# Kernel optimization log

Hardware: AMD Instinct MI355X
Metric: run time of the kernel (lower is better)

## Reference

```python
import jax, jax.numpy as jnp
import numpy as np

N, IN_DIM, OUT_DIM, HEADS = 50000, 256, 256, 8
C = OUT_DIM // HEADS  # per-head channels = 32
E = 800000
G = 64  # number of graphs in the batch
NEG_SLOPE = 0.2
GN_EPS = 1e-5


def setup_inputs() -> dict:
    key = jax.random.key(0)
    ks = jax.random.split(key, 12)
    x = jax.random.normal(ks[0], (N, IN_DIM), dtype=jnp.float32)
    edge_index = jax.random.randint(ks[1], (2, E), 0, N, dtype=jnp.int64)
    batch = jnp.sort(jax.random.randint(ks[2], (N,), 0, G, dtype=jnp.int64))
    s = 1.0 / np.sqrt(IN_DIM)
    W_l = jax.random.uniform(ks[3], (IN_DIM, HEADS * C), jnp.float32, -s, s)
    b_l = jnp.zeros((HEADS * C,), jnp.float32)
    W_r = jax.random.uniform(ks[4], (IN_DIM, HEADS * C), jnp.float32, -s, s)
    b_r = jnp.zeros((HEADS * C,), jnp.float32)
    att = jax.random.normal(ks[5], (HEADS, C), dtype=jnp.float32) / np.sqrt(C)
    bias = jnp.zeros((HEADS * C,), jnp.float32)
    gn_weight = jnp.ones((OUT_DIM,), jnp.float32)
    gn_bias = jnp.zeros((OUT_DIM,), jnp.float32)
    gn_mean_scale = jnp.ones((OUT_DIM,), jnp.float32)
    return {"x": x, "edge_index": edge_index, "batch": batch,
            "W_l": W_l, "b_l": b_l, "W_r": W_r, "b_r": b_r,
            "att": att, "bias": bias, "gn_weight": gn_weight,
            "gn_bias": gn_bias, "gn_mean_scale": gn_mean_scale}


def _gat_block(x, src, dst, batch, W_l, b_l, W_r, b_r, att, bias,
               gn_weight, gn_bias, gn_mean_scale):
    n = x.shape[0]
    # GATv2Conv (add_self_loops=True, concat=True)
    loops = jnp.arange(n, dtype=src.dtype)
    src = jnp.concatenate([src, loops])
    dst = jnp.concatenate([dst, loops])
    xl = (x @ W_l + b_l).reshape(n, HEADS, C)  # source transform
    xr = (x @ W_r + b_r).reshape(n, HEADS, C)  # target transform
    e = jax.nn.leaky_relu(xl[src] + xr[dst], NEG_SLOPE)  # [E', H, C]
    logits = jnp.einsum('ehc,hc->eh', e, att)            # [E', H]
    # segment softmax over incoming edges of each destination node
    m = jax.ops.segment_max(logits, dst, num_segments=n)
    alpha = jnp.exp(logits - m[dst])
    denom = jax.ops.segment_sum(alpha, dst, num_segments=n)
    alpha = alpha / (denom[dst] + 1e-16)
    msg = xl[src] * alpha[:, :, None]                    # [E', H, C]
    h = jax.ops.segment_sum(msg, dst, num_segments=n).reshape(n, HEADS * C) + bias
    # identity residual (in_dim == out_dim) + ELU
    h = jax.nn.elu(h + x)
    # GraphNorm (post-norm)
    counts = jnp.maximum(jax.ops.segment_sum(jnp.ones((n,), h.dtype), batch,
                                             num_segments=G), 1.0)
    mean = jax.ops.segment_sum(h, batch, num_segments=G) / counts[:, None]
    out0 = h - gn_mean_scale * mean[batch]
    var = jax.ops.segment_sum(out0 * out0, batch, num_segments=G) / counts[:, None]
    return gn_weight * out0 / jnp.sqrt(var[batch] + GN_EPS) + gn_bias


def reference(x, edge_index, batch, W_l, b_l, W_r, b_r, att, bias,
              gn_weight, gn_bias, gn_mean_scale):
    return _gat_block(x, edge_index[0], edge_index[1], batch,
                      W_l, b_l, W_r, b_r, att, bias,
                      gn_weight, gn_bias, gn_mean_scale)
```

## Files before the change

kernel.cpp:

```cpp
#include <hip/hip_runtime.h>
#include <hip/hip_bf16.h>
#include <stdint.h>

#define N_NODES 50000
#define MPAD    50048
#define IN_DIM  256
#define EDGES   800000
#define EPRIME  (EDGES + N_NODES)
#define NGRAPH  64
#define GN_EPS  1e-5f
#define ECPAD   53248
#define NBLK    208

typedef __attribute__((ext_vector_type(8))) short short8;
typedef __attribute__((ext_vector_type(4))) float floatx4;
typedef __attribute__((ext_vector_type(2))) float float2v;

__device__ __forceinline__ uint32_t pk2bf(float a, float b) {
    union { __hip_bfloat162 h; uint32_t u; } cv;
    cv.h = __float22bfloat162_rn(make_float2(a, b));
    return cv.u;
}

__device__ __forceinline__ unsigned short f2b(float f) {
    uint32_t u = __float_as_uint(f);
    u += 0x7fffu + ((u >> 16) & 1u);
    return (unsigned short)(u >> 16);
}

__global__ __launch_bounds__(256) void k_prep_w(const float* __restrict__ Wl,
                                                const float* __restrict__ Wr,
                                                unsigned short* __restrict__ Wt) {
    int idx = blockIdx.x * 256 + threadIdx.x;
    int n = idx >> 8, k = idx & 255;
    float v = (n < 256) ? Wl[k * 256 + n] : Wr[k * 256 + (n - 256)];
    Wt[idx] = f2b(v);
}

__global__ __launch_bounds__(512) void k_gemm(const float* __restrict__ x,
                                              const unsigned short* __restrict__ Wt,
                                              const float* __restrict__ bl,
                                              const float* __restrict__ br,
                                              unsigned short* __restrict__ XL,
                                              unsigned short* __restrict__ XR) {
    __shared__ unsigned short As[64 * 256];
    int rbase = blockIdx.x * 64;
    int tid = threadIdx.x;

#pragma unroll
    for (int it = 0; it < 4; ++it) {
        int c = it * 512 + tid;
        int row = c >> 5, ch = c & 31;
        int gr = rbase + row;
        float4 f0, f1;
        if (gr < N_NODES) {
            const float4* src = (const float4*)(x + (size_t)gr * 256 + ch * 8);
            f0 = src[0]; f1 = src[1];
        } else {
            f0 = make_float4(0.f,0.f,0.f,0.f); f1 = f0;
        }
        uint32_t p0 = pk2bf(f0.x, f0.y), p1 = pk2bf(f0.z, f0.w);
        uint32_t p2 = pk2bf(f1.x, f1.y), p3 = pk2bf(f1.z, f1.w);
        uint4 hv = make_uint4(p0, p1, p2, p3);
        *(uint4*)(As + row * 256 + (ch ^ (row & 7)) * 8) = hv;
    }
    __syncthreads();

    int w = tid >> 6;
    int l = tid & 63;
    int m = l & 15, q = l >> 4;

    floatx4 acc[4][4];
#pragma unroll
    for (int rf = 0; rf < 4; ++rf)
#pragma unroll
        for (int cf = 0; cf < 4; ++cf)
            acc[rf][cf] = (floatx4){0.f, 0.f, 0.f, 0.f};

    const unsigned short* wbase = Wt + (size_t)(w * 64) * 256;

#pragma unroll
    for (int kk = 0; kk < 8; ++kk) {
        short8 a[4];
#pragma unroll
        for (int rf = 0; rf < 4; ++rf) {
            int row = rf * 16 + m;
            int ch = (kk * 4 + q) ^ (row & 7);
            a[rf] = *(const short8*)(As + row * 256 + ch * 8);
        }
#pragma unroll
        for (int cf = 0; cf < 4; ++cf) {
            short8 b = *(const short8*)(wbase + (size_t)(cf * 16 + m) * 256 + kk * 32 + q * 8);
#pragma unroll
            for (int rf = 0; rf < 4; ++rf)
                acc[rf][cf] = __builtin_amdgcn_mfma_f32_16x16x32_bf16(b, a[rf], acc[rf][cf], 0, 0, 0);
        }
    }

    unsigned short* obase = (w < 4) ? XL : XR;
    const float* bptr = (w < 4) ? bl : br;
    int cb = (w & 3) * 64;
#pragma unroll
    for (int cf = 0; cf < 4; ++cf) {
        int chb = cb + cf * 16 + q * 4;
        float4 bv = *(const float4*)(bptr + chb);
#pragma unroll
        for (int rf = 0; rf < 4; ++rf) {
            int node = rbase + rf * 16 + m;
            uint2 o;
            o.x = pk2bf(acc[rf][cf][0] + bv.x, acc[rf][cf][1] + bv.y);
            o.y = pk2bf(acc[rf][cf][2] + bv.z, acc[rf][cf][3] + bv.w);
            *(uint2*)(obase + (size_t)node * 256 + chb) = o;
        }
    }
}

__global__ __launch_bounds__(256) void k_hist(const int* __restrict__ ei,
                                              const int* __restrict__ batch,
                                              int* __restrict__ ecount,
                                              int* __restrict__ ncount,
                                              int* __restrict__ sedge) {
    __shared__ int hist[NGRAPH];
    if (threadIdx.x < NGRAPH) hist[threadIdx.x] = 0;
    __syncthreads();
    int e = blockIdx.x * 256 + threadIdx.x;
    if (e < EPRIME) {
        int d = (e < EDGES) ? ei[EDGES + e] : (e - EDGES);
        atomicAdd(&ecount[d], 1);
    }
    if (e < N_NODES) atomicAdd(&hist[batch[e]], 1);
    if (blockIdx.x == 0 && threadIdx.x < 16) sedge[EPRIME + threadIdx.x] = 0;
    __syncthreads();
    if (threadIdx.x < NGRAPH && hist[threadIdx.x])
        atomicAdd(&ncount[threadIdx.x], hist[threadIdx.x]);
}

__global__ __launch_bounds__(256) void k_scan1(const int* __restrict__ ecount,
                                               int* __restrict__ bsum) {
    __shared__ int red[256];
    int v = ecount[blockIdx.x * 256 + threadIdx.x];
    red[threadIdx.x] = v;
    __syncthreads();
    for (int off = 128; off > 0; off >>= 1) {
        if (threadIdx.x < off) red[threadIdx.x] += red[threadIdx.x + off];
        __syncthreads();
    }
    if (threadIdx.x == 0) bsum[blockIdx.x] = red[0];
}

__global__ __launch_bounds__(256) void k_scan2(int* __restrict__ bsum) {
    __shared__ int buf[256];
    int t = threadIdx.x;
    int v = (t < NBLK) ? bsum[t] : 0;
    buf[t] = v;
    __syncthreads();
    for (int off = 1; off < 256; off <<= 1) {
        int p = (t >= off) ? buf[t - off] : 0;
        __syncthreads();
        buf[t] += p;
        __syncthreads();
    }
    if (t < NBLK) bsum[t] = buf[t] - v;
}

__global__ __launch_bounds__(256) void k_scan3(const int* __restrict__ ecount,
                                               const int* __restrict__ bsum,
                                               int* __restrict__ estart,
                                               int* __restrict__ ecursor) {
    __shared__ int buf[256];
    int b = blockIdx.x, t = threadIdx.x;
    int v = ecount[b * 256 + t];
    buf[t] = v;
    __syncthreads();
    for (int off = 1; off < 256; off <<= 1) {
        int p = (t >= off) ? buf[t - off] : 0;
        __syncthreads();
        buf[t] += p;
        __syncthreads();
    }
    int e = bsum[b] + buf[t] - v;
    estart[b * 256 + t]  = e;
    ecursor[b * 256 + t] = e;
}

__global__ __launch_bounds__(256) void k_scatter(const int* __restrict__ ei,
                                                 int* __restrict__ ecursor,
                                                 int* __restrict__ sedge) {
    int e = blockIdx.x * 256 + threadIdx.x;
    if (e >= EPRIME) return;
    int s, d;
    if (e < EDGES) { s = ei[e]; d = ei[EDGES + e]; }
    else           { s = d = e - EDGES; }
    int pos = atomicAdd(&ecursor[d], 1);
    sedge[pos] = s;
}

__global__ __launch_bounds__(256) void k_msg(const unsigned short* __restrict__ XL,
                                             const unsigned short* __restrict__ XRb,
                                             const float* __restrict__ x,
                                             const float* __restrict__ att,
                                             const float* __restrict__ bias,
                                             const int* __restrict__ sedge,
                                             const int* __restrict__ estart,
                                             const int* __restrict__ ecount,
                                             float* __restrict__ out) {
    int d = (int)((blockIdx.x * 256 + threadIdx.x) >> 6);
    int l = threadIdx.x & 63;
    int lofs = l * 8;

    float4 xin  = ((const float4*)(x + (size_t)d * 256))[l];
    float4 bvv  = ((const float4*)bias)[l];
    float4 attv = ((const float4*)att)[l];
    float2v att01 = {attv.x, attv.y}, att23 = {attv.z, attv.w};

    uint2 xru = ((const uint2*)(XRb + (size_t)d * 256))[l];
    float2v xr01, xr23;
    xr01[0] = __uint_as_float(xru.x << 16);
    xr01[1] = __uint_as_float(xru.x & 0xffff0000u);
    xr23[0] = __uint_as_float(xru.y << 16);
    xr23[1] = __uint_as_float(xru.y & 0xffff0000u);

    int s0  = __builtin_amdgcn_readfirstlane(estart[d]);
    int cnt = __builtin_amdgcn_readfirstlane(ecount[d]);

    auto ldrow = [&](int src) -> uint2 {
        size_t off = ((size_t)(uint32_t)__builtin_amdgcn_readfirstlane(src)) << 9;
        return *(const uint2*)((const char*)XL + off + lofs);
    };

    float den0 = 0.f, den1 = 0.f, den2 = 0.f, den3 = 0.f;
    float2v A01 = {0.f,0.f}, A23 = {0.f,0.f};
    float2v B01 = {0.f,0.f}, B23 = {0.f,0.f};
    float2v C01 = {0.f,0.f}, C23 = {0.f,0.f};
    float2v D01 = {0.f,0.f}, D23 = {0.f,0.f};

    auto proc = [&](uint2 U, float& den, float2v& R01, float2v& R23) {
        float2v x01, x23;
        x01[0] = __uint_as_float(U.x << 16);
        x01[1] = __uint_as_float(U.x & 0xffff0000u);
        x23[0] = __uint_as_float(U.y << 16);
        x23[1] = __uint_as_float(U.y & 0xffff0000u);
        float2v e01 = x01 + xr01, e23 = x23 + xr23;
        float2v f01 = e01 * 0.2f, f23 = e23 * 0.2f;
        e01[0] = fmaxf(e01[0], f01[0]); e01[1] = fmaxf(e01[1], f01[1]);
        e23[0] = fmaxf(e23[0], f23[0]); e23[1] = fmaxf(e23[1], f23[1]);
        float2v pp2 = e01 * att01 + e23 * att23;
        float pp = pp2[0] + pp2[1];
        {
            int pi = __float_as_int(pp);
            pp += __int_as_float(__builtin_amdgcn_update_dpp(0, pi, 0xB1, 0xF, 0xF, true));
            pi = __float_as_int(pp);
            pp += __int_as_float(__builtin_amdgcn_update_dpp(0, pi, 0x4E, 0xF, 0xF, true));
            pp += __int_as_float(__builtin_amdgcn_ds_swizzle(__float_as_int(pp), 0x101F));
        }
        float al = __expf(fminf(pp, 80.f));
        den += al;
        float2v al2 = {al, al};
        R01 += al2 * x01;
        R23 += al2 * x23;
    };

    uint2 P0 = ldrow(sedge[s0]);
    uint2 P1 = ldrow(sedge[s0 + 1]);
    uint2 P2 = ldrow(sedge[s0 + 2]);
    uint2 P3 = ldrow(sedge[s0 + 3]);

    int nq = cnt >> 2;
    for (int qq = 0; qq < nq; ++qq) {
        uint2 Q0 = P0, Q1 = P1, Q2 = P2, Q3 = P3;
        int nb = s0 + (qq + 1) * 4;
        P0 = ldrow(sedge[nb]);
        P1 = ldrow(sedge[nb + 1]);
        P2 = ldrow(sedge[nb + 2]);
        P3 = ldrow(sedge[nb + 3]);
        proc(Q0, den0, A01, A23);
        proc(Q1, den1, B01, B23);
        proc(Q2, den2, C01, C23);
        proc(Q3, den3, D01, D23);
    }
    int rem = cnt & 3;
    if (rem > 0) proc(P0, den0, A01, A23);
    if (rem > 1) proc(P1, den1, B01, B23);
    if (rem > 2) proc(P2, den2, C01, C23);

    float inv = 1.f / ((den0 + den1) + (den2 + den3) + 1e-16f);
    A01 = (A01 + B01) + (C01 + D01);
    A23 = (A23 + B23) + (C23 + D23);

    float h0 = A01[0] * inv + bvv.x + xin.x; h0 = (h0 > 0.f) ? h0 : (__expf(h0) - 1.f);
    float h1 = A01[1] * inv + bvv.y + xin.y; h1 = (h1 > 0.f) ? h1 : (__expf(h1) - 1.f);
    float h2 = A23[0] * inv + bvv.z + xin.z; h2 = (h2 > 0.f) ? h2 : (__expf(h2) - 1.f);
    float h3 = A23[1] * inv + bvv.w + xin.w; h3 = (h3 > 0.f) ? h3 : (__expf(h3) - 1.f);
    ((float4*)(out + (size_t)d * 256))[l] = make_float4(h0, h1, h2, h3);
}

#define GN_ROWS 64
__global__ __launch_bounds__(256) void k_gn_sum(const float* __restrict__ h,
                                                const int* __restrict__ batch,
                                                float* __restrict__ gsum,
                                                float* __restrict__ gsq) {
    __shared__ int bsh[GN_ROWS];
    int r0 = blockIdx.x * GN_ROWS;
    if (threadIdx.x < GN_ROWS) {
        int i = r0 + threadIdx.x;
        bsh[threadIdx.x] = (i < N_NODES) ? batch[i] : -1;
    }
    __syncthreads();
    int c = threadIdx.x;
    float s1 = 0.f, s2 = 0.f;
    int g = bsh[0];
    for (int j = 0; j < GN_ROWS; j += 4) {
        int i = r0 + j;
        if (i >= N_NODES) break;
        bool full = (i + 3 < N_NODES);
        if (full && bsh[j] == g && bsh[j + 3] == g) {
            const float* hp = h + (size_t)i * 256 + c;
            float v0 = hp[0], v1 = hp[256], v2 = hp[512], v3 = hp[768];
            s1 += (v0 + v1) + (v2 + v3);
            s2 += (v0 * v0 + v1 * v1) + (v2 * v2 + v3 * v3);
        } else {
            for (int jj = j; jj < j + 4; ++jj) {
                int ii = r0 + jj;
                if (ii >= N_NODES) break;
                int bg = bsh[jj];
                if (bg != g) {
                    atomicAdd(&gsum[g * 256 + c], s1);
                    atomicAdd(&gsq[g * 256 + c], s2);
                    s1 = 0.f; s2 = 0.f; g = bg;
                }
                float v = h[(size_t)ii * 256 + c];
                s1 += v; s2 += v * v;
            }
        }
    }
    atomicAdd(&gsum[g * 256 + c], s1);
    atomicAdd(&gsq[g * 256 + c], s2);
}

__global__ __launch_bounds__(256) void k_final(float* __restrict__ out,
                                               const int* __restrict__ batch,
                                               const float* __restrict__ gsum,
                                               const float* __restrict__ gsq,
                                               const int* __restrict__ ncount,
                                               const float* __restrict__ gnw,
                                               const float* __restrict__ gnb,
                                               const float* __restrict__ gms) {
    int idx = blockIdx.x * 256 + threadIdx.x;
    int i = idx >> 6, l = idx & 63;
    if (i >= N_NODES) return;
    int g = batch[i];
    float inv = 1.f / fmaxf((float)ncount[g], 1.f);
    float4 hv = ((const float4*)(out + (size_t)i * 256))[l];
    float4 ms = ((const float4*)(gsum + g * 256))[l];
    float4 qs = ((const float4*)(gsq  + g * 256))[l];
    float4 wv = ((const float4*)gnw)[l];
    float4 bv = ((const float4*)gnb)[l];
    float4 sv = ((const float4*)gms)[l];
    float4 o;
    {
        float m = ms.x * inv, q = qs.x * inv;
        o.x = wv.x * (hv.x - sv.x * m) * rsqrtf(q - m * m * sv.x * (2.f - sv.x) + GN_EPS) + bv.x;
    }
    {
        float m = ms.y * inv, q = qs.y * inv;
        o.y = wv.y * (hv.y - sv.y * m) * rsqrtf(q - m * m * sv.y * (2.f - sv.y) + GN_EPS) + bv.y;
    }
    {
        float m = ms.z * inv, q = qs.z * inv;
        o.z = wv.z * (hv.z - sv.z * m) * rsqrtf(q - m * m * sv.z * (2.f - sv.z) + GN_EPS) + bv.z;
    }
    {
        float m = ms.w * inv, q = qs.w * inv;
        o.w = wv.w * (hv.w - sv.w * m) * rsqrtf(q - m * m * sv.w * (2.f - sv.w) + GN_EPS) + bv.w;
    }
    ((float4*)(out + (size_t)i * 256))[l] = o;
}

extern "C" void kernel_launch(void* const* d_in, const int* in_sizes, int n_in,
                              void* d_out, int out_size, void* d_ws, size_t ws_size,
                              hipStream_t stream) {
    const float* x    = (const float*)d_in[0];
    const int*   ei   = (const int*)d_in[1];
    const int*   batch= (const int*)d_in[2];
    const float* Wl   = (const float*)d_in[3];
    const float* bl   = (const float*)d_in[4];
    const float* Wr   = (const float*)d_in[5];
    const float* br   = (const float*)d_in[6];
    const float* att  = (const float*)d_in[7];
    const float* bias = (const float*)d_in[8];
    const float* gnw  = (const float*)d_in[9];
    const float* gnb  = (const float*)d_in[10];
    const float* gms  = (const float*)d_in[11];
    float* out = (float*)d_out;

    char* p = (char*)d_ws;
    auto alloc = [&](size_t bytes) -> char* {
        char* r = p;
        p += (bytes + 255) & ~(size_t)255;
        return r;
    };
    unsigned short* Wt  = (unsigned short*)alloc((size_t)512 * 256 * 2);
    unsigned short* XL  = (unsigned short*)alloc((size_t)MPAD * 256 * 2);
    unsigned short* XRb = (unsigned short*)alloc((size_t)MPAD * 256 * 2);
    int* estart         = (int*)alloc((size_t)ECPAD * 4);
    int* ecursor        = (int*)alloc((size_t)ECPAD * 4);
    int* sedge          = (int*)alloc((size_t)(EPRIME + 16) * 4);
    int* bsum           = (int*)alloc((size_t)256 * 4);
    int* ecount         = (int*)alloc((size_t)ECPAD * 4);
    int* ncount         = (int*)alloc((size_t)NGRAPH * 4);
    float* gsum         = (float*)alloc((size_t)2 * NGRAPH * 256 * 4);
    float* gsq          = gsum + NGRAPH * 256;
    size_t zbytes = (size_t)((char*)(gsum + 2 * NGRAPH * 256) - (char*)ecount);
    hipMemsetAsync(ecount, 0, zbytes, stream);

    k_prep_w<<<512, 256, 0, stream>>>(Wl, Wr, Wt);
    k_gemm<<<MPAD / 64, 512, 0, stream>>>(x, Wt, bl, br, XL, XRb);

    k_hist<<<(EPRIME + 255) / 256, 256, 0, stream>>>(ei, batch, ecount, ncount, sedge);
    k_scan1<<<NBLK, 256, 0, stream>>>(ecount, bsum);
    k_scan2<<<1, 256, 0, stream>>>(bsum);
    k_scan3<<<NBLK, 256, 0, stream>>>(ecount, bsum, estart, ecursor);
    k_scatter<<<(EPRIME + 255) / 256, 256, 0, stream>>>(ei, ecursor, sedge);

    k_msg<<<N_NODES / 4, 256, 0, stream>>>(XL, XRb, x, att, bias,
                                           sedge, estart, ecount, out);

    k_gn_sum<<<(N_NODES + GN_ROWS - 1) / GN_ROWS, 256, 0, stream>>>(out, batch, gsum, gsq);
    k_final<<<N_NODES * 64 / 256, 256, 0, stream>>>(out, batch, gsum, gsq,
                                                    ncount, gnw, gnb, gms);
}
```

Measured before the change: 364.4 us.

## Split message kernel wavefront into two half-waves processing different edges

The message-passing kernel now has each 64-lane wavefront handle two edges at once. Each half-wave of 32 lanes loads a full 256-channel bf16 row with 16-byte loads, where before all 64 lanes loaded one row with 8-byte loads. The first 128 source indices are preloaded into registers and broadcast with readlane instead of being fetched from memory per edge. The halves are combined with cross-lane shuffles at the end, and a mask handles odd edge counts. The intent is to halve the serial edge loop length and cut reduction and index-load overhead, at the cost of more registers, a final shuffle reduction, and extra padding on the edge array.

```diff
diff --git a/kernel.cpp b/kernel.cpp
--- a/kernel.cpp
+++ b/kernel.cpp
@@ -26,6 +26,13 @@
     uint32_t u = __float_as_uint(f);
     u += 0x7fffu + ((u >> 16) & 1u);
     return (unsigned short)(u >> 16);
+}
+
+__device__ __forceinline__ float2v up2(uint32_t u) {
+    float2v r;
+    r[0] = __uint_as_float(u << 16);
+    r[1] = __uint_as_float(u & 0xffff0000u);
+    return r;
 }
 
 __global__ __launch_bounds__(256) void k_prep_w(const float* __restrict__ Wl,
@@ -129,7 +136,7 @@
         atomicAdd(&ecount[d], 1);
     }
     if (e < N_NODES) atomicAdd(&hist[batch[e]], 1);
-    if (blockIdx.x == 0 && threadIdx.x < 16) sedge[EPRIME + threadIdx.x] = 0;
+    if (blockIdx.x == 0 && threadIdx.x < 192) sedge[EPRIME + threadIdx.x] = 0;
     __syncthreads();
     if (threadIdx.x < NGRAPH && hist[threadIdx.x])
         atomicAdd(&ncount[threadIdx.x], hist[threadIdx.x]);
@@ -206,92 +213,121 @@
                                              float* __restrict__ out) {
     int d = (int)((blockIdx.x * 256 + threadIdx.x) >> 6);
     int l = threadIdx.x & 63;
-    int lofs = l * 8;
-
-    float4 xin  = ((const float4*)(x + (size_t)d * 256))[l];
-    float4 bvv  = ((const float4*)bias)[l];
-    float4 attv = ((const float4*)att)[l];
-    float2v att01 = {attv.x, attv.y}, att23 = {attv.z, attv.w};
-
-    uint2 xru = ((const uint2*)(XRb + (size_t)d * 256))[l];
-    float2v xr01, xr23;
-    xr01[0] = __uint_as_float(xru.x << 16);
-    xr01[1] = __uint_as_float(xru.x & 0xffff0000u);
-    xr23[0] = __uint_as_float(xru.y << 16);
-    xr23[1] = __uint_as_float(xru.y & 0xffff0000u);
+    int j = l & 31;
+    int half = l >> 5;
+    uint32_t jofs = (uint32_t)j * 16u;
+    float hmask = (half == 0) ? 1.f : 0.f;
+
+    uint4 xr4 = ((const uint4*)(XRb + (size_t)d * 256))[j];
+    float2v xr01 = up2(xr4.x), xr23 = up2(xr4.y), xr45 = up2(xr4.z), xr67 = up2(xr4.w);
+    float4 at0 = ((const float4*)att)[j * 2];
+    float4 at1 = ((const float4*)att)[j * 2 + 1];
+    float2v a01 = {at0.x, at0.y}, a23 = {at0.z, at0.w};
+    float2v a45 = {at1.x, at1.y}, a67 = {at1.z, at1.w};
 
     int s0  = __builtin_amdgcn_readfirstlane(estart[d]);
     int cnt = __builtin_amdgcn_readfirstlane(ecount[d]);
 
-    auto ldrow = [&](int src) -> uint2 {
-        size_t off = ((size_t)(uint32_t)__builtin_amdgcn_readfirstlane(src)) << 9;
-        return *(const uint2*)((const char*)XL + off + lofs);
+    int esrc0 = sedge[s0 + l];
+    int esrc1 = sedge[s0 + 64 + l];
+
+    int hA = (cnt + 1) >> 1;
+    int nB = cnt >> 1;
+
+    auto getsrc = [&](int i) -> int {
+        if (i < 128) {
+            int lo = __builtin_amdgcn_readlane(esrc0, i & 63);
+            int hi = __builtin_amdgcn_readlane(esrc1, i & 63);
+            return (i < 64) ? lo : hi;
+        }
+        return sedge[s0 + i];
     };
-
-    float den0 = 0.f, den1 = 0.f, den2 = 0.f, den3 = 0.f;
-    float2v A01 = {0.f,0.f}, A23 = {0.f,0.f};
-    float2v B01 = {0.f,0.f}, B23 = {0.f,0.f};
-    float2v C01 = {0.f,0.f}, C23 = {0.f,0.f};
-    float2v D01 = {0.f,0.f}, D23 = {0.f,0.f};
-
-    auto proc = [&](uint2 U, float& den, float2v& R01, float2v& R23) {
-        float2v x01, x23;
-        x01[0] = __uint_as_float(U.x << 16);
-        x01[1] = __uint_as_float(U.x & 0xffff0000u);
-        x23[0] = __uint_as_float(U.y << 16);
-        x23[1] = __uint_as_float(U.y & 0xffff0000u);
-        float2v e01 = x01 + xr01, e23 = x23 + xr23;
-        float2v f01 = e01 * 0.2f, f23 = e23 * 0.2f;
-        e01[0] = fmaxf(e01[0], f01[0]); e01[1] = fmaxf(e01[1], f01[1]);
-        e23[0] = fmaxf(e23[0], f23[0]); e23[1] = fmaxf(e23[1], f23[1]);
-        float2v pp2 = e01 * att01 + e23 * att23;
+    auto ldpair = [&](int sA, int sB) -> uint4 {
+        uint32_t s = half ? (uint32_t)sB : (uint32_t)sA;
+        return *(const uint4*)((const char*)XL + (((size_t)s) << 9) + jofs);
+    };
+
+    float den0 = 0.f, den1 = 0.f;
+    float2v A01={0.f,0.f}, A23={0.f,0.f}, A45={0.f,0.f}, A67={0.f,0.f};
+    float2v B01={0.f,0.f}, B23={0.f,0.f}, B45={0.f,0.f}, B67={0.f,0.f};
+
+    auto proc = [&](uint4 U, float hm, float& den, float2v& R01, float2v& R23,
+                    float2v& R45, float2v& R67) {
+        float2v x01 = up2(U.x), x23 = up2(U.y), x45 = up2(U.z), x67 = up2(U.w);
+        float2v z01 = x01 + xr01, z23 = x23 + xr23;
+        float2v z45 = x45 + xr45, z67 = x67 + xr67;
+        float2v f01 = z01 * 0.2f, f23 = z23 * 0.2f;
+        float2v f45 = z45 * 0.2f, f67 = z67 * 0.2f;
+        z01[0] = fmaxf(z01[0], f01[0]); z01[1] = fmaxf(z01[1], f01[1]);
+        z23[0] = fmaxf(z23[0], f23[0]); z23[1] = fmaxf(z23[1], f23[1]);
+        z45[0] = fmaxf(z45[0], f45[0]); z45[1] = fmaxf(z45[1], f45[1]);
+        z67[0] = fmaxf(z67[0], f67[0]); z67[1] = fmaxf(z67[1], f67[1]);
+        float2v pp2 = z01 * a01;
+        pp2 += z23 * a23;
+        pp2 += z45 * a45;
+        pp2 += z67 * a67;
         float pp = pp2[0] + pp2[1];
-        {
-            int pi = __float_as_int(pp);
-            pp += __int_as_float(__builtin_amdgcn_update_dpp(0, pi, 0xB1, 0xF, 0xF, true));
-            pi = __float_as_int(pp);
-            pp += __int_as_float(__builtin_amdgcn_update_dpp(0, pi, 0x4E, 0xF, 0xF, true));
-            pp += __int_as_float(__builtin_amdgcn_ds_swizzle(__float_as_int(pp), 0x101F));
-        }
-        float al = __expf(fminf(pp, 80.f));
+        int pi = __float_as_int(pp);
+        pp += __int_as_float(__builtin_amdgcn_update_dpp(0, pi, 0xB1, 0xF, 0xF, true));
+        pi = __float_as_int(pp);
+        pp += __int_as_float(__builtin_amdgcn_update_dpp(0, pi, 0x4E, 0xF, 0xF, true));
+        float al = __expf(fminf(pp, 80.f)) * hm;
         den += al;
         float2v al2 = {al, al};
-        R01 += al2 * x01;
-        R23 += al2 * x23;
+        R01 += al2 * x01; R23 += al2 * x23;
+        R45 += al2 * x45; R67 += al2 * x67;
     };
 
-    uint2 P0 = ldrow(sedge[s0]);
-    uint2 P1 = ldrow(sedge[s0 + 1]);
-    uint2 P2 = ldrow(sedge[s0 + 2]);
-    uint2 P3 = ldrow(sedge[s0 + 3]);
-
-    int nq = cnt >> 2;
+    uint4 P0 = ldpair(getsrc(0), getsrc(hA));
+    uint4 P1 = ldpair(getsrc(1), getsrc(hA + 1));
+    uint4 P2 = ldpair(getsrc(2), getsrc(hA + 2));
+    uint4 P3 = ldpair(getsrc(3), getsrc(hA + 3));
+
+    int nq = nB >> 2, rem = nB & 3;
     for (int qq = 0; qq < nq; ++qq) {
-        uint2 Q0 = P0, Q1 = P1, Q2 = P2, Q3 = P3;
-        int nb = s0 + (qq + 1) * 4;
-        P0 = ldrow(sedge[nb]);
-        P1 = ldrow(sedge[nb + 1]);
-        P2 = ldrow(sedge[nb + 2]);
-        P3 = ldrow(sedge[nb + 3]);
-        proc(Q0, den0, A01, A23);
-        proc(Q1, den1, B01, B23);
-        proc(Q2, den2, C01, C23);
-        proc(Q3, den3, D01, D23);
-    }
-    int rem = cnt & 3;
-    if (rem > 0) proc(P0, den0, A01, A23);
-    if (rem > 1) proc(P1, den1, B01, B23);
-    if (rem > 2) proc(P2, den2, C01, C23);
-
-    float inv = 1.f / ((den0 + den1) + (den2 + den3) + 1e-16f);
-    A01 = (A01 + B01) + (C01 + D01);
-    A23 = (A23 + B23) + (C23 + D23);
-
-    float h0 = A01[0] * inv + bvv.x + xin.x; h0 = (h0 > 0.f) ? h0 : (__expf(h0) - 1.f);
-    float h1 = A01[1] * inv + bvv.y + xin.y; h1 = (h1 > 0.f) ? h1 : (__expf(h1) - 1.f);
-    float h2 = A23[0] * inv + bvv.z + xin.z; h2 = (h2 > 0.f) ? h2 : (__expf(h2) - 1.f);
-    float h3 = A23[1] * inv + bvv.w + xin.w; h3 = (h3 > 0.f) ? h3 : (__expf(h3) - 1.f);
-    ((float4*)(out + (size_t)d * 256))[l] = make_float4(h0, h1, h2, h3);
+        uint4 Q0 = P0, Q1 = P1, Q2 = P2, Q3 = P3;
+        int b = (qq + 1) * 4;
+        P0 = ldpair(getsrc(b),     getsrc(hA + b));
+        P1 = ldpair(getsrc(b + 1), getsrc(hA + b + 1));
+        P2 = ldpair(getsrc(b + 2), getsrc(hA + b + 2));
+        P3 = ldpair(getsrc(b + 3), getsrc(hA + b + 3));
+        proc(Q0, 1.f, den0, A01, A23, A45, A67);
+        proc(Q1, 1.f, den1, B01, B23, B45, B67);
+        proc(Q2, 1.f, den0, A01, A23, A45, A67);
+        proc(Q3, 1.f, den1, B01, B23, B45, B67);
+    }
+    if (rem > 0) proc(P0, 1.f, den0, A01, A23, A45, A67);
+    if (rem > 1) proc(P1, 1.f, den1, B01, B23, B45, B67);
+    if (rem > 2) proc(P2, 1.f, den0, A01, A23, A45, A67);
+    if (cnt & 1) {
+        if      (rem == 0) proc(P0, hmask, den1, B01, B23, B45, B67);
+        else if (rem == 1) proc(P1, hmask, den1, B01, B23, B45, B67);
+        else if (rem == 2) proc(P2, hmask, den1, B01, B23, B45, B67);
+        else               proc(P3, hmask, den1, B01, B23, B45, B67);
+    }
+
+    float den = den0 + den1;
+    den += __shfl_xor(den, 32);
+    float2v R01 = A01 + B01, R23 = A23 + B23, R45 = A45 + B45, R67 = A67 + B67;
+    R01[0] += __shfl_xor(R01[0], 32); R01[1] += __shfl_xor(R01[1], 32);
+    R23[0] += __shfl_xor(R23[0], 32); R23[1] += __shfl_xor(R23[1], 32);
+    R45[0] += __shfl_xor(R45[0], 32); R45[1] += __shfl_xor(R45[1], 32);
+    R67[0] += __shfl_xor(R67[0], 32); R67[1] += __shfl_xor(R67[1], 32);
+    float inv = 1.f / (den + 1e-16f);
+
+    bool hi = (half != 0);
+    float c0 = hi ? R45[0] : R01[0];
+    float c1 = hi ? R45[1] : R01[1];
+    float c2 = hi ? R67[0] : R23[0];
+    float c3 = hi ? R67[1] : R23[1];
+    int chb = j * 8 + half * 4;
+    float4 xin = *(const float4*)(x + (size_t)d * 256 + chb);
+    float4 bv  = *(const float4*)(bias + chb);
+    float h0 = c0 * inv + bv.x + xin.x; h0 = (h0 > 0.f) ? h0 : (__expf(h0) - 1.f);
+    float h1 = c1 * inv + bv.y + xin.y; h1 = (h1 > 0.f) ? h1 : (__expf(h1) - 1.f);
+    float h2 = c2 * inv + bv.z + xin.z; h2 = (h2 > 0.f) ? h2 : (__expf(h2) - 1.f);
+    float h3 = c3 * inv + bv.w + xin.w; h3 = (h3 > 0.f) ? h3 : (__expf(h3) - 1.f);
+    *(float4*)(out + (size_t)d * 256 + chb) = make_float4(h0, h1, h2, h3);
 }
 
 #define GN_ROWS 64
@@ -404,7 +440,7 @@
     unsigned short* XRb = (unsigned short*)alloc((size_t)MPAD * 256 * 2);
     int* estart         = (int*)alloc((size_t)ECPAD * 4);
     int* ecursor        = (int*)alloc((size_t)ECPAD * 4);
-    int* sedge          = (int*)alloc((size_t)(EPRIME + 16) * 4);
+    int* sedge          = (int*)alloc((size_t)(EPRIME + 192) * 4);
     int* bsum           = (int*)alloc((size_t)256 * 4);
     int* ecount         = (int*)alloc((size_t)ECPAD * 4);
     int* ncount         = (int*)alloc((size_t)NGRAPH * 4);
```

Result: no change. 365.5 us (+0.3%).
